# Kernel tuning notes

Hardware: AMD Instinct MI355X
Metric: run time of the kernel (lower is better)

Reference implementation:

```python
import jax, jax.numpy as jnp
import numpy as np

D = 256          # common_dim = specific_dim
NH = 8           # num_heads
HD = D // NH     # head_dim = 32
B, S = 16, 1024
EPS = 1e-5


def _mha(q, k, v, wq, bq, wk, bk, wv, bv, wo, bo):
    # q,k,v: [B, S, D]; weights stored [in, out] so y = x @ w + b
    b_, _, _ = q.shape

    def proj(x, w, b):
        return (x @ w + b).reshape(b_, -1, NH, HD).transpose(0, 2, 1, 3)  # [B,H,S,hd]

    Q, K, V = proj(q, wq, bq), proj(k, wk, bk), proj(v, wv, bv)
    scores = jnp.einsum('bhqd,bhkd->bhqk', Q, K) / (float(HD) ** 0.5)
    attn = jax.nn.softmax(scores, axis=-1)
    out = jnp.einsum('bhqk,bhkd->bhqd', attn, V)
    out = out.transpose(0, 2, 1, 3).reshape(b_, -1, D)
    return out @ wo + bo


def _ln(x, g, b):
    mu = jnp.mean(x, axis=-1, keepdims=True)
    var = jnp.var(x, axis=-1, keepdims=True)
    return (x - mu) * jax.lax.rsqrt(var + EPS) * g + b


def setup_inputs() -> dict:
    key = jax.random.key(0)
    ks = iter(jax.random.split(key, 32))
    rn = lambda *shape: jax.random.normal(next(ks), shape, dtype=jnp.float32)
    w = lambda i, o: rn(i, o) * 0.05
    inp = {
        'img_common': rn(B, S, D),
        'txt_common': rn(B, S, D),
        'img_specific': rn(B, D),
        'txt_specific': rn(B, D),
    }
    for pfx in ('i2t', 't2i'):
        for nm in ('q', 'k', 'v', 'o'):
            inp[f'{pfx}_w{nm}'] = w(D, D)
            inp[f'{pfx}_b{nm}'] = jnp.zeros((D,), jnp.float32)
    inp['ln_img_g'] = jnp.ones((D,), jnp.float32)
    inp['ln_img_b'] = jnp.zeros((D,), jnp.float32)
    inp['ln_txt_g'] = jnp.ones((D,), jnp.float32)
    inp['ln_txt_b'] = jnp.zeros((D,), jnp.float32)
    inp['enh_w'] = w(2 * D, D)
    inp['enh_b'] = jnp.zeros((D,), jnp.float32)
    inp['inc_w'] = w(2 * D, D)
    inp['inc_b'] = jnp.zeros((D,), jnp.float32)
    return inp


def reference(img_common, txt_common, img_specific, txt_specific,
              i2t_wq, i2t_bq, i2t_wk, i2t_bk, i2t_wv, i2t_bv, i2t_wo, i2t_bo,
              t2i_wq, t2i_bq, t2i_wk, t2i_bk, t2i_wv, t2i_bv, t2i_wo, t2i_bo,
              ln_img_g, ln_img_b, ln_txt_g, ln_txt_b,
              enh_w, enh_b, inc_w, inc_b):
    att_i2t = _mha(img_common, txt_common, txt_common,
                   i2t_wq, i2t_bq, i2t_wk, i2t_bk, i2t_wv, i2t_bv, i2t_wo, i2t_bo)
    img_query = _ln(att_i2t + img_common, ln_img_g, ln_img_b)
    att_t2i = _mha(txt_common, img_common, img_common,
                   t2i_wq, t2i_bq, t2i_wk, t2i_bk, t2i_wv, t2i_bv, t2i_wo, t2i_bo)
    txt_query = _ln(att_t2i + txt_common, ln_txt_g, ln_txt_b)
    combined = jnp.concatenate((img_query, txt_query), axis=-1)  # [B,S,2D]
    enhancement = combined @ enh_w + enh_b                        # [B,S,D]
    inc = jnp.concatenate((img_specific - txt_specific,
                           img_specific * txt_specific), axis=1)  # [B,2D]
    inconsistency = inc @ inc_w + inc_b                           # [B,D]
    return (enhancement, inconsistency, img_specific, txt_specific)
```

## Files before the change

kernel.cpp:

```cpp
#include <hip/hip_runtime.h>
#include <stdint.h>

typedef unsigned int u32;
typedef unsigned short u16;
typedef __attribute__((ext_vector_type(8))) short bf16x8;
typedef __attribute__((ext_vector_type(4))) float f32x4;

#define BUF_ELEMS (16384 * 256)

__device__ __forceinline__ float bflo(u32 u) { return __uint_as_float(u << 16); }
__device__ __forceinline__ float bfhi(u32 u) { return __uint_as_float(u & 0xffff0000u); }
__device__ __forceinline__ u16 f2bf(float f) {
    u32 u = __float_as_uint(f);
    return (u16)((u + 0x7fffu + ((u >> 16) & 1u)) >> 16);
}
__device__ __forceinline__ u32 pkhi(float lo, float hi) {
    return __builtin_amdgcn_perm(__float_as_uint(hi), __float_as_uint(lo), 0x07060302u);
}

struct WT {
    const float* src[9];
    u16* dst[9];
    const float* bs[6];
    float* bA;
    float* bB;
    const float* img_sp;
    const float* txt_sp;
    const float* incw;
    const float* incb;
    float* out_inc;
    float* out_img;
    float* out_txt;
};

__global__ __launch_bounds__(256)
void wtrans_kernel(WT wt)
{
    __shared__ float T[64][65];
    const int bid = blockIdx.x, t = threadIdx.x;
    if (bid == 160) {
        wt.bA[t]       = wt.bs[0][t];
        wt.bA[256 + t] = wt.bs[1][t];
        wt.bA[512 + t] = wt.bs[2][t];
        wt.bB[t]       = wt.bs[3][t];
        wt.bB[256 + t] = wt.bs[4][t];
        wt.bB[512 + t] = wt.bs[5][t];
        return;
    }
    if (bid > 160) {
        float* iv = &T[0][0];
        const int b = bid - 161, n = t;
        float a = wt.img_sp[b * 256 + n];
        float x = wt.txt_sp[b * 256 + n];
        iv[n] = a - x;
        iv[256 + n] = a * x;
        __syncthreads();
        float acc = wt.incb[n];
        for (int k = 0; k < 512; k++) acc += iv[k] * wt.incw[k * 256 + n];
        wt.out_inc[b * 256 + n] = acc;
        wt.out_img[b * 256 + n] = a;
        wt.out_txt[b * 256 + n] = x;
        return;
    }
    int m, sub;
    if (bid < 128) { m = bid >> 4; sub = bid & 15; }
    else           { m = 8;        sub = bid - 128; }
    const int K = (m == 8) ? 512 : 256;
    const int kt = (m == 8) ? (sub & 7) : (sub & 3);
    const int nt = (m == 8) ? (sub >> 3) : (sub >> 2);
    const int k0 = kt * 64, n0 = nt * 64;
    const float* src = wt.src[m];
    u16* dst = wt.dst[m];

    const int kk = t >> 2, nn = (t & 3) * 16;
    #pragma unroll
    for (int j = 0; j < 16; j += 4) {
        float4 v = *(const float4*)(src + (size_t)(k0 + kk) * 256 + n0 + nn + j);
        T[kk][nn + j + 0] = v.x; T[kk][nn + j + 1] = v.y;
        T[kk][nn + j + 2] = v.z; T[kk][nn + j + 3] = v.w;
    }
    __syncthreads();
    const int nn2 = t >> 2, kc = (t & 3) * 16;
    #pragma unroll
    for (int j = 0; j < 16; j++)
        dst[(size_t)(n0 + nn2) * K + k0 + kc + j] = f2bf(T[kc + j][nn2]);
}

template<int MODE>
__global__ __launch_bounds__(256)
void gemm_mfma(const float* __restrict__ Af0, const float* __restrict__ Af1,
               const u16* __restrict__ Ab0, const u16* __restrict__ Ab1,
               const u16* __restrict__ Wt0, const u16* __restrict__ Wt1,
               const float* __restrict__ bias0, const float* __restrict__ bias1,
               void* __restrict__ o0, void* __restrict__ o1, void* __restrict__ o2,
               void* __restrict__ o3, void* __restrict__ o4, void* __restrict__ o5)
{
    __shared__ u16 As[128][72];
    __shared__ u16 Bs[128][72];
    const int tid = threadIdx.x;
    const int wave = tid >> 6, lane = tid & 63;
    const int L = lane & 15, Qd = lane >> 4;
    int m_idx, n_idx;
    if (MODE == 0)      { m_idx = blockIdx.x & 255; n_idx = blockIdx.x >> 8; }
    else if (MODE == 1) { m_idx = blockIdx.x & 255; n_idx = blockIdx.x >> 8; }
    else                { m_idx = blockIdx.x & 127; n_idx = blockIdx.x >> 7; }
    const bool msel = (MODE != 2) && (m_idx >= 128 * (MODE == 0 ? 1 : 1) && MODE == 0
                       ? (m_idx >= 128) : (MODE == 1 && m_idx >= 128));
    const bool ms = (MODE == 0 || MODE == 1) ? (m_idx >= 128) : false;
    const int lm0 = (MODE == 2) ? m_idx * 128 : (m_idx & 127) * 128;
    const int n0 = n_idx * 128;
    const u16* Wt = ms ? Wt1 : Wt0;
    const float* bias = ms ? bias1 : bias0;
    const int wr = wave & 1, wc = wave >> 1;
    const int sr = tid >> 1, sh = (tid & 1) * 32;
    const int KS = (MODE == 2) ? 512 : 256;
    (void)msel;

    f32x4 acc[4][4] = {};

    for (int kt = 0; kt < KS; kt += 64) {
        if (MODE == 0) {
            const float* Af = ms ? Af1 : Af0;
            const float* Ap = Af + (size_t)(lm0 + sr) * 256 + kt + sh;
            uint4 pk[2];
            #pragma unroll
            for (int half = 0; half < 2; half++) {
                float4 f0 = *(const float4*)(Ap + half * 16);
                float4 f1 = *(const float4*)(Ap + half * 16 + 4);
                float4 f2 = *(const float4*)(Ap + half * 16 + 8);
                float4 f3 = *(const float4*)(Ap + half * 16 + 12);
                pk[half].x = pkhi(f0.x, f0.y);
                pk[half].y = pkhi(f0.z, f0.w);
                pk[half].z = pkhi(f1.x, f1.y);
                pk[half].w = pkhi(f1.z, f1.w);
                uint4 q;
                q.x = pkhi(f2.x, f2.y); q.y = pkhi(f2.z, f2.w);
                q.z = pkhi(f3.x, f3.y); q.w = pkhi(f3.z, f3.w);
                *(uint4*)&As[sr][sh + half * 16 + 8] = q;
            }
            *(uint4*)&As[sr][sh + 0] = pk[0];
            *(uint4*)&As[sr][sh + 16] = pk[1];
        } else {
            const u16* Abase;
            int lkt = kt;
            if (MODE == 2) { Abase = (kt < 256) ? Ab0 : Ab1; lkt = kt & 255; }
            else           { Abase = ms ? Ab1 : Ab0; }
            const u16* Ap = Abase + (size_t)(lm0 + sr) * 256 + lkt + sh;
            uint4 a0 = *(const uint4*)(Ap + 0);
            uint4 a1 = *(const uint4*)(Ap + 8);
            uint4 a2 = *(const uint4*)(Ap + 16);
            uint4 a3 = *(const uint4*)(Ap + 24);
            *(uint4*)&As[sr][sh + 0]  = a0;
            *(uint4*)&As[sr][sh + 8]  = a1;
            *(uint4*)&As[sr][sh + 16] = a2;
            *(uint4*)&As[sr][sh + 24] = a3;
        }
        {
            const u16* Bp = Wt + (size_t)(n0 + sr) * KS + kt + sh;
            uint4 w0 = *(const uint4*)(Bp + 0);
            uint4 w1 = *(const uint4*)(Bp + 8);
            uint4 w2 = *(const uint4*)(Bp + 16);
            uint4 w3 = *(const uint4*)(Bp + 24);
            *(uint4*)&Bs[sr][sh + 0]  = w0;
            *(uint4*)&Bs[sr][sh + 8]  = w1;
            *(uint4*)&Bs[sr][sh + 16] = w2;
            *(uint4*)&Bs[sr][sh + 24] = w3;
        }
        __syncthreads();
        #pragma unroll
        for (int kh = 0; kh < 64; kh += 32) {
            bf16x8 af[4], bf[4];
            #pragma unroll
            for (int mt = 0; mt < 4; mt++)
                af[mt] = *(const bf16x8*)&As[wr * 64 + mt * 16 + L][kh + Qd * 8];
            #pragma unroll
            for (int nt = 0; nt < 4; nt++)
                bf[nt] = *(const bf16x8*)&Bs[wc * 64 + nt * 16 + L][kh + Qd * 8];
            #pragma unroll
            for (int mt = 0; mt < 4; mt++)
                #pragma unroll
                for (int nt = 0; nt < 4; nt++)
                    acc[mt][nt] = __builtin_amdgcn_mfma_f32_16x16x32_bf16(
                        af[mt], bf[nt], acc[mt][nt], 0, 0, 0);
        }
        __syncthreads();
    }

    float bvals[4];
    #pragma unroll
    for (int nt = 0; nt < 4; nt++)
        bvals[nt] = bias[n0 + wc * 64 + nt * 16 + L];

    const float qsc = (MODE == 0 && n_idx < 2)
                      ? (0.17677669529663687f * 1.4426950408889634f) : 1.0f;

    void* outp;
    int colb;
    if (MODE == 0) {
        const int g = n_idx >> 1;
        if (!ms) outp = (g == 0) ? o0 : ((g == 1) ? o1 : o2);
        else     outp = (g == 0) ? o3 : ((g == 1) ? o4 : o5);
        colb = (n_idx & 1) * 128 + wc * 64;
    } else if (MODE == 1) {
        outp = ms ? o1 : o0;
        colb = n0 + wc * 64;
    } else {
        outp = o0;
        colb = n0 + wc * 64;
    }
    #pragma unroll
    for (int mt = 0; mt < 4; mt++) {
        #pragma unroll
        for (int r = 0; r < 4; r++) {
            const size_t row = (size_t)(lm0 + wr * 64 + mt * 16 + Qd * 4 + r) * 256;
            #pragma unroll
            for (int nt = 0; nt < 4; nt++) {
                const int col = colb + nt * 16 + L;
                float v = (acc[mt][nt][r] + bvals[nt]) * qsc;
                if (MODE == 2) ((float*)outp)[row + col] = v;
                else           ((u16*)outp)[row + col] = f2bf(v);
            }
        }
    }
}

__global__ __launch_bounds__(256, 4)
void attn_mfma(const u16* __restrict__ Q0, const u16* __restrict__ K0,
               const u16* __restrict__ V0, u16* __restrict__ O0,
               const u16* __restrict__ Q1, const u16* __restrict__ K1,
               const u16* __restrict__ V1, u16* __restrict__ O1)
{
    __shared__ u16 Ks[128][40];
    __shared__ u16 Vt[32][136];
    __shared__ u16 Ps[4][16][136];
    const int tid = threadIdx.x;
    const int wave = tid >> 6, lane = tid & 63;
    const int L = lane & 15, Qd = lane >> 4;
    const int bid = blockIdx.x;
    const int qt = bid >> 8;
    const int kv = bid & 255;
    const int set = kv >> 7;
    const int b = (kv >> 3) & 15;
    const int h = kv & 7;
    const u16* Q = set ? Q1 : Q0;
    const u16* K = set ? K1 : K0;
    const u16* V = set ? V1 : V0;
    u16* O = set ? O1 : O0;
    const int rowbase = b * 1024;
    const int qbase = rowbase + qt * 128;

    bf16x8 qfrag[2];
    #pragma unroll
    for (int qs = 0; qs < 2; qs++)
        qfrag[qs] = *(const bf16x8*)(Q + (size_t)(qbase + qs * 64 + wave * 16 + L) * 256
                                       + h * 32 + Qd * 8);

    const short oneb = (short)0x3F80;
    const bf16x8 ones = {oneb, oneb, oneb, oneb, oneb, oneb, oneb, oneb};

    f32x4 oacc[2][2] = {};
    f32x4 oaccL[2] = {};

    const int sr = tid >> 1;
    const int scol = (tid & 1) * 16;
    const int vcol = (sr & 15) * 8 + (sr >> 4);

    for (int t = 0; t < 8; t++) {
        const size_t kvbase = (size_t)(rowbase + t * 128 + sr) * 256 + h * 32 + scol;
        uint4 k1 = *(const uint4*)(K + kvbase);
        uint4 k2 = *(const uint4*)(K + kvbase + 8);
        uint4 v1 = *(const uint4*)(V + kvbase);
        uint4 v2 = *(const uint4*)(V + kvbase + 8);
        *(uint4*)&Ks[sr][scol]     = k1;
        *(uint4*)&Ks[sr][scol + 8] = k2;
        union { uint4 u4[2]; u16 us[16]; } vv;
        vv.u4[0] = v1; vv.u4[1] = v2;
        #pragma unroll
        for (int j = 0; j < 16; j++) Vt[scol + j][vcol] = vv.us[j];
        __syncthreads();

        bf16x8 kf[8];
        #pragma unroll
        for (int ct = 0; ct < 8; ct++)
            kf[ct] = *(const bf16x8*)&Ks[ct * 16 + L][Qd * 8];

        #pragma unroll
        for (int qs = 0; qs < 2; qs++) {
            const f32x4 z = {0.f, 0.f, 0.f, 0.f};
            f32x4 sacc[8];
            #pragma unroll
            for (int ct = 0; ct < 8; ct++)
                sacc[ct] = __builtin_amdgcn_mfma_f32_16x16x32_bf16(qfrag[qs], kf[ct], z, 0, 0, 0);
            #pragma unroll
            for (int r = 0; r < 4; r++) {
                float p[8];
                #pragma unroll
                for (int ct = 0; ct < 8; ct++) p[ct] = exp2f(sacc[ct][r]);
                uint4 pk;
                pk.x = pkhi(p[0], p[1]);
                pk.y = pkhi(p[2], p[3]);
                pk.z = pkhi(p[4], p[5]);
                pk.w = pkhi(p[6], p[7]);
                *(uint4*)&Ps[wave][Qd * 4 + r][L * 8] = pk;
            }
            #pragma unroll
            for (int kc = 0; kc < 4; kc++) {
                bf16x8 pfrag = *(const bf16x8*)&Ps[wave][L][kc * 32 + Qd * 8];
                bf16x8 vf0 = *(const bf16x8*)&Vt[L][kc * 32 + Qd * 8];
                bf16x8 vf1 = *(const bf16x8*)&Vt[16 + L][kc * 32 + Qd * 8];
                oacc[qs][0] = __builtin_amdgcn_mfma_f32_16x16x32_bf16(pfrag, vf0, oacc[qs][0], 0, 0, 0);
                oacc[qs][1] = __builtin_amdgcn_mfma_f32_16x16x32_bf16(pfrag, vf1, oacc[qs][1], 0, 0, 0);
                oaccL[qs]   = __builtin_amdgcn_mfma_f32_16x16x32_bf16(pfrag, ones, oaccL[qs], 0, 0, 0);
            }
        }
        __syncthreads();
    }

    #pragma unroll
    for (int qs = 0; qs < 2; qs++) {
        #pragma unroll
        for (int r = 0; r < 4; r++) {
            float inv = 1.f / oaccL[qs][r];
            const size_t orow = (size_t)(qbase + qs * 64 + wave * 16 + Qd * 4 + r) * 256 + h * 32;
            O[orow + L]      = f2bf(oacc[qs][0][r] * inv);
            O[orow + 16 + L] = f2bf(oacc[qs][1][r] * inv);
        }
    }
}

__global__ __launch_bounds__(256)
void ln_res_kernel(const u16* __restrict__ P0, const u16* __restrict__ P1,
                   const float* __restrict__ R0, const float* __restrict__ R1,
                   const float* __restrict__ g0, const float* __restrict__ be0,
                   const float* __restrict__ g1, const float* __restrict__ be1,
                   u16* __restrict__ out0, u16* __restrict__ out1)
{
    const int lane = threadIdx.x & 63;
    int row = blockIdx.x * 4 + (threadIdx.x >> 6);
    const bool sel = row >= 16384;
    const u16* P = sel ? P1 : P0;
    const float* R = sel ? R1 : R0;
    const float* g = sel ? g1 : g0;
    const float* be = sel ? be1 : be0;
    u16* out = sel ? out1 : out0;
    if (sel) row -= 16384;
    const int col = lane * 4;
    uint2 pv = *(const uint2*)(P + (size_t)row * 256 + col);
    float4 rv = *(const float4*)(R + (size_t)row * 256 + col);
    float x0 = bflo(pv.x) + rv.x;
    float x1 = bfhi(pv.x) + rv.y;
    float x2 = bflo(pv.y) + rv.z;
    float x3 = bfhi(pv.y) + rv.w;
    float s = x0 + x1 + x2 + x3;
    float s2 = x0*x0 + x1*x1 + x2*x2 + x3*x3;
    #pragma unroll
    for (int off = 32; off > 0; off >>= 1) {
        s  += __shfl_xor(s, off);
        s2 += __shfl_xor(s2, off);
    }
    float mean = s * 0.00390625f;
    float var = fmaxf(s2 * 0.00390625f - mean * mean, 0.f);
    float rstd = rsqrtf(var + 1e-5f);
    float4 gv = *(const float4*)(g + col);
    float4 bv = *(const float4*)(be + col);
    uint2 pk;
    pk.x = (u32)f2bf((x0 - mean) * rstd * gv.x + bv.x)
         | ((u32)f2bf((x1 - mean) * rstd * gv.y + bv.y) << 16);
    pk.y = (u32)f2bf((x2 - mean) * rstd * gv.z + bv.z)
         | ((u32)f2bf((x3 - mean) * rstd * gv.w + bv.w) << 16);
    *(uint2*)(out + (size_t)row * 256 + col) = pk;
}

extern "C" void kernel_launch(void* const* d_in, const int* in_sizes, int n_in,
                              void* d_out, int out_size, void* d_ws, size_t ws_size,
                              hipStream_t stream)
{
    (void)in_sizes; (void)n_in; (void)out_size; (void)ws_size;
    const float* img    = (const float*)d_in[0];
    const float* txt    = (const float*)d_in[1];
    const float* img_sp = (const float*)d_in[2];
    const float* txt_sp = (const float*)d_in[3];
    const float* wq_i = (const float*)d_in[4];  const float* bq_i = (const float*)d_in[5];
    const float* wk_i = (const float*)d_in[6];  const float* bk_i = (const float*)d_in[7];
    const float* wv_i = (const float*)d_in[8];  const float* bv_i = (const float*)d_in[9];
    const float* wo_i = (const float*)d_in[10]; const float* bo_i = (const float*)d_in[11];
    const float* wq_t = (const float*)d_in[12]; const float* bq_t = (const float*)d_in[13];
    const float* wk_t = (const float*)d_in[14]; const float* bk_t = (const float*)d_in[15];
    const float* wv_t = (const float*)d_in[16]; const float* bv_t = (const float*)d_in[17];
    const float* wo_t = (const float*)d_in[18]; const float* bo_t = (const float*)d_in[19];
    const float* lng_i = (const float*)d_in[20]; const float* lnb_i = (const float*)d_in[21];
    const float* lng_t = (const float*)d_in[22]; const float* lnb_t = (const float*)d_in[23];
    const float* enh_w = (const float*)d_in[24]; const float* enh_b = (const float*)d_in[25];
    const float* incw  = (const float*)d_in[26]; const float* incb  = (const float*)d_in[27];
    float* out = (float*)d_out;
    u16* wsp = (u16*)d_ws;
    u16* B0 = wsp;
    u16* B1 = wsp + 1 * (size_t)BUF_ELEMS;
    u16* B2 = wsp + 2 * (size_t)BUF_ELEMS;
    u16* B3 = wsp + 3 * (size_t)BUF_ELEMS;
    u16* B4 = wsp + 4 * (size_t)BUF_ELEMS;
    u16* B5 = wsp + 5 * (size_t)BUF_ELEMS;
    u16* wbase = wsp + 6 * (size_t)BUF_ELEMS;
    u16* WtA   = wbase;
    u16* WtB   = wbase + 196608;
    u16* Wt_oi = wbase + 393216;
    u16* Wt_ot = wbase + 458752;
    u16* Wt_en = wbase + 524288;
    float* biasA = (float*)(wbase + 655360);
    float* biasB = biasA + 768;

    dim3 blk(256);
    WT wt;
    wt.src[0] = wq_i; wt.dst[0] = WtA;
    wt.src[1] = wk_t; wt.dst[1] = WtA + 65536;
    wt.src[2] = wv_t; wt.dst[2] = WtA + 131072;
    wt.src[3] = wq_t; wt.dst[3] = WtB;
    wt.src[4] = wk_i; wt.dst[4] = WtB + 65536;
    wt.src[5] = wv_i; wt.dst[5] = WtB + 131072;
    wt.src[6] = wo_i; wt.dst[6] = Wt_oi;
    wt.src[7] = wo_t; wt.dst[7] = Wt_ot;
    wt.src[8] = enh_w; wt.dst[8] = Wt_en;
    wt.bs[0] = bq_i; wt.bs[1] = bk_t; wt.bs[2] = bv_t;
    wt.bs[3] = bq_t; wt.bs[4] = bk_i; wt.bs[5] = bv_i;
    wt.bA = biasA; wt.bB = biasB;
    wt.img_sp = img_sp; wt.txt_sp = txt_sp; wt.incw = incw; wt.incb = incb;
    wt.out_inc = out + 4194304; wt.out_img = out + 4198400; wt.out_txt = out + 4202496;
    wtrans_kernel<<<177, blk, 0, stream>>>(wt);

    gemm_mfma<0><<<1536, blk, 0, stream>>>(img, txt, nullptr, nullptr,
                                           WtA, WtB, biasA, biasB,
                                           B0, B4, B5, B3, B1, B2);
    attn_mfma<<<2048, blk, 0, stream>>>(B0, B1, B2, B0, B3, B4, B5, B3);
    gemm_mfma<1><<<512, blk, 0, stream>>>(nullptr, nullptr, B0, B3,
                                          Wt_oi, Wt_ot, bo_i, bo_t,
                                          B1, B4, nullptr, nullptr, nullptr, nullptr);
    ln_res_kernel<<<8192, blk, 0, stream>>>(B1, B4, img, txt,
                                            lng_i, lnb_i, lng_t, lnb_t, B2, B5);
    gemm_mfma<2><<<256, blk, 0, stream>>>(nullptr, nullptr, B2, B5,
                                          Wt_en, nullptr, enh_b, nullptr,
                                          out, nullptr, nullptr, nullptr, nullptr, nullptr);
}
```

Baseline: 308.4 us.

## Store V head-transposed from projection GEMM and prefetch K/V in attention

```diff
diff --git a/kernel.cpp b/kernel.cpp
--- a/kernel.cpp
+++ b/kernel.cpp
@@ -16,6 +16,20 @@
 }
 __device__ __forceinline__ u32 pkhi(float lo, float hi) {
     return __builtin_amdgcn_perm(__float_as_uint(hi), __float_as_uint(lo), 0x07060302u);
+}
+__device__ __forceinline__ float fexp2(float x) {
+#if __has_builtin(__builtin_amdgcn_exp2f)
+    return __builtin_amdgcn_exp2f(x);
+#else
+    float r; asm("v_exp_f32 %0, %1" : "=v"(r) : "v"(x)); return r;
+#endif
+}
+__device__ __forceinline__ float frcp(float x) {
+#if __has_builtin(__builtin_amdgcn_rcpf)
+    return __builtin_amdgcn_rcpf(x);
+#else
+    return 1.f / x;
+#endif
 }
 
 struct WT {
@@ -104,8 +118,6 @@
     if (MODE == 0)      { m_idx = blockIdx.x & 255; n_idx = blockIdx.x >> 8; }
     else if (MODE == 1) { m_idx = blockIdx.x & 255; n_idx = blockIdx.x >> 8; }
     else                { m_idx = blockIdx.x & 127; n_idx = blockIdx.x >> 7; }
-    const bool msel = (MODE != 2) && (m_idx >= 128 * (MODE == 0 ? 1 : 1) && MODE == 0
-                       ? (m_idx >= 128) : (MODE == 1 && m_idx >= 128));
     const bool ms = (MODE == 0 || MODE == 1) ? (m_idx >= 128) : false;
     const int lm0 = (MODE == 2) ? m_idx * 128 : (m_idx & 127) * 128;
     const int n0 = n_idx * 128;
@@ -114,7 +126,6 @@
     const int wr = wave & 1, wc = wave >> 1;
     const int sr = tid >> 1, sh = (tid & 1) * 32;
     const int KS = (MODE == 2) ? 512 : 256;
-    (void)msel;
 
     f32x4 acc[4][4] = {};
 
@@ -208,6 +219,29 @@
         outp = o0;
         colb = n0 + wc * 64;
     }
+
+    if (MODE == 0 && n_idx >= 4) {
+        u16* Vg = (u16*)outp;
+        #pragma unroll
+        for (int mt = 0; mt < 4; mt++) {
+            const int tokb = lm0 + wr * 64 + mt * 16 + Qd * 4;
+            const int b_ = tokb >> 10;
+            const int s_ = tokb & 1023;
+            #pragma unroll
+            for (int nt = 0; nt < 4; nt++) {
+                const int col = colb + nt * 16 + L;
+                const int h_ = col >> 5, d_ = col & 31;
+                uint2 pk2;
+                pk2.x = (u32)f2bf(acc[mt][nt][0] + bvals[nt])
+                      | ((u32)f2bf(acc[mt][nt][1] + bvals[nt]) << 16);
+                pk2.y = (u32)f2bf(acc[mt][nt][2] + bvals[nt])
+                      | ((u32)f2bf(acc[mt][nt][3] + bvals[nt]) << 16);
+                *(uint2*)(Vg + ((size_t)((b_ * 8 + h_) * 32 + d_) << 10) + s_) = pk2;
+            }
+        }
+        return;
+    }
+
     #pragma unroll
     for (int mt = 0; mt < 4; mt++) {
         #pragma unroll
@@ -261,23 +295,38 @@
     f32x4 oacc[2][2] = {};
     f32x4 oaccL[2] = {};
 
-    const int sr = tid >> 1;
-    const int scol = (tid & 1) * 16;
-    const int vcol = (sr & 15) * 8 + (sr >> 4);
+    const int kkey  = tid >> 1;
+    const int kcolh = (tid & 1) * 16;
+    const int krow  = (kkey & 7) * 16 + (kkey >> 3);
+    const int vd    = tid >> 3;
+    const int vkb   = (tid & 7) * 16;
+    const size_t vplane = (size_t)((b * 8 + h) * 32 + vd) * 1024;
+
+    uint4 kr0, kr1, vr0, vr1;
+    {
+        const size_t kb = (size_t)(rowbase + kkey) * 256 + h * 32 + kcolh;
+        kr0 = *(const uint4*)(K + kb);
+        kr1 = *(const uint4*)(K + kb + 8);
+        const size_t vb = vplane + vkb;
+        vr0 = *(const uint4*)(V + vb);
+        vr1 = *(const uint4*)(V + vb + 8);
+    }
 
     for (int t = 0; t < 8; t++) {
-        const size_t kvbase = (size_t)(rowbase + t * 128 + sr) * 256 + h * 32 + scol;
-        uint4 k1 = *(const uint4*)(K + kvbase);
-        uint4 k2 = *(const uint4*)(K + kvbase + 8);
-        uint4 v1 = *(const uint4*)(V + kvbase);
-        uint4 v2 = *(const uint4*)(V + kvbase + 8);
-        *(uint4*)&Ks[sr][scol]     = k1;
-        *(uint4*)&Ks[sr][scol + 8] = k2;
-        union { uint4 u4[2]; u16 us[16]; } vv;
-        vv.u4[0] = v1; vv.u4[1] = v2;
-        #pragma unroll
-        for (int j = 0; j < 16; j++) Vt[scol + j][vcol] = vv.us[j];
+        *(uint4*)&Ks[krow][kcolh]     = kr0;
+        *(uint4*)&Ks[krow][kcolh + 8] = kr1;
+        *(uint4*)&Vt[vd][vkb]         = vr0;
+        *(uint4*)&Vt[vd][vkb + 8]     = vr1;
         __syncthreads();
+
+        if (t < 7) {
+            const size_t kb = (size_t)(rowbase + (t + 1) * 128 + kkey) * 256 + h * 32 + kcolh;
+            kr0 = *(const uint4*)(K + kb);
+            kr1 = *(const uint4*)(K + kb + 8);
+            const size_t vb = vplane + (t + 1) * 128 + vkb;
+            vr0 = *(const uint4*)(V + vb);
+            vr1 = *(const uint4*)(V + vb + 8);
+        }
 
         bf16x8 kf[8];
         #pragma unroll
@@ -295,7 +344,7 @@
             for (int r = 0; r < 4; r++) {
                 float p[8];
                 #pragma unroll
-                for (int ct = 0; ct < 8; ct++) p[ct] = exp2f(sacc[ct][r]);
+                for (int ct = 0; ct < 8; ct++) p[ct] = fexp2(sacc[ct][r]);
                 uint4 pk;
                 pk.x = pkhi(p[0], p[1]);
                 pk.y = pkhi(p[2], p[3]);
@@ -320,7 +369,7 @@
     for (int qs = 0; qs < 2; qs++) {
         #pragma unroll
         for (int r = 0; r < 4; r++) {
-            float inv = 1.f / oaccL[qs][r];
+            float inv = frcp(oaccL[qs][r]);
             const size_t orow = (size_t)(qbase + qs * 64 + wave * 16 + Qd * 4 + r) * 256 + h * 32;
             O[orow + L]      = f2bf(oacc[qs][0][r] * inv);
             O[orow + 16 + L] = f2bf(oacc[qs][1][r] * inv);
```

After: 292.7 us. 1.05x faster.
